# Kernel optimization log

Measured on AMD Instinct MI355X. Metric: run time of the kernel, lower is better.

The kernel has to match this reference:

```python
import jax, jax.numpy as jnp
import numpy as np

B, S = 32, 1
NUM_Q_HEADS, NUM_KV_HEADS, HEAD_DIM = 4, 2, 64
HIDDEN = NUM_Q_HEADS * HEAD_DIM          # 256
QKV_DIM = HIDDEN + 2 * NUM_KV_HEADS * HEAD_DIM  # 512
MAX_SEQ = 8192
G = NUM_Q_HEADS // NUM_KV_HEADS          # q heads per kv head


def setup_inputs() -> dict:
    key = jax.random.key(0)
    ks = jax.random.split(key, 6)
    x = jax.random.normal(ks[0], (B, S, HIDDEN), dtype=jnp.float32)
    kv_cache = jax.random.normal(ks[1], (B, 2, NUM_KV_HEADS, MAX_SEQ, HEAD_DIM), dtype=jnp.float32)
    ctx_len_tensor = jax.random.randint(ks[2], (B,), 0, 8000, dtype=jnp.int32)
    # RoPE table: [MAX_SEQ, HEAD_DIM] = [cos | sin] over half-dim
    half = HEAD_DIM // 2
    inv_freq = 1.0 / (10000.0 ** (np.arange(half, dtype=np.float32) / half))
    ang = np.arange(MAX_SEQ, dtype=np.float32)[:, None] * inv_freq[None, :]
    rope = jnp.asarray(np.concatenate([np.cos(ang), np.sin(ang)], axis=-1), dtype=jnp.float32)
    qkv_w = jax.random.normal(ks[3], (QKV_DIM, HIDDEN), dtype=jnp.float32) * (HIDDEN ** -0.5)
    qkv_b = jax.random.normal(ks[4], (QKV_DIM,), dtype=jnp.float32) * 0.02
    out_w = jax.random.normal(ks[5], (HIDDEN, HIDDEN), dtype=jnp.float32) * (HIDDEN ** -0.5)
    return {"x": x, "kv_cache": kv_cache, "ctx_len_tensor": ctx_len_tensor,
            "rope": rope, "qkv_w": qkv_w, "qkv_b": qkv_b, "out_w": out_w}


def reference(x, kv_cache, ctx_len_tensor, rope, qkv_w, qkv_b, out_w):
    b, s, _ = x.shape
    hd, half = HEAD_DIM, HEAD_DIM // 2
    qkv = jnp.einsum('bsd,ed->bse', x, qkv_w) + qkv_b
    q = qkv[..., :HIDDEN].reshape(b, s, NUM_Q_HEADS, hd)
    k = qkv[..., HIDDEN:HIDDEN + NUM_KV_HEADS * hd].reshape(b, s, NUM_KV_HEADS, hd)
    v = qkv[..., HIDDEN + NUM_KV_HEADS * hd:].reshape(b, s, NUM_KV_HEADS, hd)

    # positions of the new tokens in the cache
    pos = ctx_len_tensor[:, None] + jnp.arange(s)           # [b, s]
    cos = rope[pos, :half][:, :, None, :]                    # [b, s, 1, half]
    sin = rope[pos, half:][:, :, None, :]

    def rot(t):
        t1, t2 = t[..., :half], t[..., half:]
        return jnp.concatenate([t1 * cos - t2 * sin, t1 * sin + t2 * cos], axis=-1)

    q = rot(q)
    k = rot(k)

    # scatter new k/v into cache at pos (one-hot, positions distinct within batch)
    m = jnp.arange(MAX_SEQ)
    onehot = (m[None, None, :] == pos[:, :, None]).astype(kv_cache.dtype)   # [b, s, M]
    written = onehot.sum(axis=1)                                            # [b, M]
    keep = (1.0 - written)[:, None, :, None]                                # [b, 1, M, 1]
    cache_k = kv_cache[:, 0] * keep + jnp.einsum('bsm,bshd->bhmd', onehot, k)
    cache_v = kv_cache[:, 1] * keep + jnp.einsum('bsm,bshd->bhmd', onehot, v)

    # GQA decode attention over the updated cache (causal w.r.t. absolute position)
    qg = q.reshape(b, s, NUM_KV_HEADS, G, hd)
    scale = hd ** -0.5
    scores = jnp.einsum('bskgd,bkmd->bskgm', qg, cache_k) * scale           # [b,s,Hkv,G,M]
    valid = (m[None, None, :] <= pos[:, :, None])[:, :, None, None, :]
    scores = jnp.where(valid, scores, jnp.finfo(scores.dtype).min)
    attn = jax.nn.softmax(scores, axis=-1)
    ctx = jnp.einsum('bskgm,bkmd->bskgd', attn, cache_v).reshape(b, s, HIDDEN)

    out = jnp.einsum('bsd,ed->bse', ctx, out_w)
    updated_kv = jnp.stack([cache_k, cache_v], axis=1)
    return out, updated_kv
```

## Files before the change

### kernel.cpp

```cpp
#include <hip/hip_runtime.h>
#include <math.h>

#define B 32
#define NQH 4
#define NKVH 2
#define HD 64
#define HIDDEN 256
#define QKV_DIM 512
#define MAX_SEQ 8192
#define PLANE (MAX_SEQ * HD)
#define SCALE 0.125f
#define CH 256
#define NCH (MAX_SEQ / CH)
#define NEG_BIG -1e30f

typedef float f4 __attribute__((ext_vector_type(4)));

#define WS_K    8192
#define WS_V    12288
#define WS_PART 16384

__global__ __launch_bounds__(256) void qkv_rope_kernel(
    const float* __restrict__ x, const int* __restrict__ ctx_len,
    const float* __restrict__ rope, const float* __restrict__ qkv_w,
    const float* __restrict__ qkv_b, float* __restrict__ ws) {
    __shared__ float sx[HIDDEN];
    __shared__ float sv[HIDDEN];
    int bb = blockIdx.x;
    int b = bb >> 1, half = bb & 1;
    int tid = threadIdx.x;
    sx[tid] = x[b * HIDDEN + tid];
    __syncthreads();
    const float4* sx4 = (const float4*)sx;
    int e = half * 256 + tid;
    const float4* wrow = (const float4*)(qkv_w + e * HIDDEN);
    float acc = 0.f;
#pragma unroll 8
    for (int d4 = 0; d4 < HIDDEN / 4; ++d4) {
        float4 w = wrow[d4], xx = sx4[d4];
        acc += w.x * xx.x + w.y * xx.y + w.z * xx.z + w.w * xx.w;
    }
    sv[tid] = acc + qkv_b[e];
    __syncthreads();
    int pos = ctx_len[b];
    int nrot = half ? 64 : 128;
    if (tid < nrot) {
        int which = tid >> 5, d = tid & 31;
        float c = rope[pos * HD + d];
        float s = rope[pos * HD + 32 + d];
        int base = which * HD;
        float t1 = sv[base + d], t2 = sv[base + 32 + d];
        sv[base + d] = t1 * c - t2 * s;
        sv[base + 32 + d] = t1 * s + t2 * c;
    }
    __syncthreads();
    if (half == 0) {
        ws[b * HIDDEN + tid] = sv[tid];
    } else if (tid < 128) {
        ws[WS_K + b * 128 + tid] = sv[tid];
    } else {
        ws[WS_V + b * 128 + (tid - 128)] = sv[tid];
    }
}

__global__ __launch_bounds__(256) void fused_copy_attn(
    const float* __restrict__ kv_cache, const int* __restrict__ ctx_len,
    const float* __restrict__ ws, float* __restrict__ out_kv,
    float* __restrict__ partials) {
    int idx = blockIdx.x;
    int chunk = idx & (NCH - 1);
    int h = (idx >> 5) & 1;
    int b = idx >> 6;
    int pos = ctx_len[b];
    int start = chunk * CH;
    int tid = threadIdx.x;
    size_t koff = ((size_t)(b * 2 + 0) * NKVH + h) * PLANE;
    size_t voff = ((size_t)(b * 2 + 1) * NKVH + h) * PLANE;
    const f4* kin = (const f4*)(kv_cache + koff);
    const f4* vin = (const f4*)(kv_cache + voff);
    f4* kout = (f4*)(out_kv + koff);
    f4* vout = (f4*)(out_kv + voff);

    if (start >= pos) {
        int base = start * 16;
#pragma unroll
        for (int i = 0; i < 16; ++i) {
            int o = base + i * 256 + tid;
            f4 k4 = __builtin_nontemporal_load(&kin[o]);
            f4 v4 = __builtin_nontemporal_load(&vin[o]);
            __builtin_nontemporal_store(k4, &kout[o]);
            __builtin_nontemporal_store(v4, &vout[o]);
        }
        return;
    }

    int w = tid >> 6, lane = tid & 63;
    int g = lane >> 4, j = lane & 15;
    float4 q0 = *(const float4*)(ws + b * HIDDEN + (h * 2 + 0) * HD + 4 * j);
    float4 q1 = *(const float4*)(ws + b * HIDDEN + (h * 2 + 1) * HD + 4 * j);
    float m0 = NEG_BIG, m1 = NEG_BIG, l0 = 0.f, l1 = 0.f;
    float4 a0 = {0, 0, 0, 0}, a1 = {0, 0, 0, 0};
#pragma unroll 4
    for (int i = 0; i < CH / 16; ++i) {
        int row = start + i * 16 + w * 4 + g;
        int fidx = row * 16 + j;
        f4 k4 = __builtin_nontemporal_load(&kin[fidx]);
        f4 v4 = __builtin_nontemporal_load(&vin[fidx]);
        __builtin_nontemporal_store(k4, &kout[fidx]);
        __builtin_nontemporal_store(v4, &vout[fidx]);
        if (row < pos) {
            float s0 = q0.x * k4[0] + q0.y * k4[1] + q0.z * k4[2] + q0.w * k4[3];
            float s1 = q1.x * k4[0] + q1.y * k4[1] + q1.z * k4[2] + q1.w * k4[3];
#pragma unroll
            for (int off = 1; off <= 8; off <<= 1) {
                s0 += __shfl_xor(s0, off);
                s1 += __shfl_xor(s1, off);
            }
            s0 *= SCALE; s1 *= SCALE;
            float nm0 = fmaxf(m0, s0);
            float al0 = __expf(m0 - nm0);
            float p0 = __expf(s0 - nm0);
            l0 = l0 * al0 + p0;
            a0.x = a0.x * al0 + p0 * v4[0]; a0.y = a0.y * al0 + p0 * v4[1];
            a0.z = a0.z * al0 + p0 * v4[2]; a0.w = a0.w * al0 + p0 * v4[3];
            m0 = nm0;
            float nm1 = fmaxf(m1, s1);
            float al1 = __expf(m1 - nm1);
            float p1 = __expf(s1 - nm1);
            l1 = l1 * al1 + p1;
            a1.x = a1.x * al1 + p1 * v4[0]; a1.y = a1.y * al1 + p1 * v4[1];
            a1.z = a1.z * al1 + p1 * v4[2]; a1.w = a1.w * al1 + p1 * v4[3];
            m1 = nm1;
        }
    }
#pragma unroll
    for (int off = 16; off <= 32; off <<= 1) {
        float om0 = __shfl_xor(m0, off), ol0 = __shfl_xor(l0, off);
        float om1 = __shfl_xor(m1, off), ol1 = __shfl_xor(l1, off);
        float4 oa0, oa1;
        oa0.x = __shfl_xor(a0.x, off); oa0.y = __shfl_xor(a0.y, off);
        oa0.z = __shfl_xor(a0.z, off); oa0.w = __shfl_xor(a0.w, off);
        oa1.x = __shfl_xor(a1.x, off); oa1.y = __shfl_xor(a1.y, off);
        oa1.z = __shfl_xor(a1.z, off); oa1.w = __shfl_xor(a1.w, off);
        float M0 = fmaxf(m0, om0);
        float ea0 = __expf(m0 - M0), eb0 = __expf(om0 - M0);
        l0 = l0 * ea0 + ol0 * eb0;
        a0.x = a0.x * ea0 + oa0.x * eb0; a0.y = a0.y * ea0 + oa0.y * eb0;
        a0.z = a0.z * ea0 + oa0.z * eb0; a0.w = a0.w * ea0 + oa0.w * eb0;
        m0 = M0;
        float M1 = fmaxf(m1, om1);
        float ea1 = __expf(m1 - M1), eb1 = __expf(om1 - M1);
        l1 = l1 * ea1 + ol1 * eb1;
        a1.x = a1.x * ea1 + oa1.x * eb1; a1.y = a1.y * ea1 + oa1.y * eb1;
        a1.z = a1.z * ea1 + oa1.z * eb1; a1.w = a1.w * ea1 + oa1.w * eb1;
        m1 = M1;
    }
    __shared__ float sm[4][2], sl[4][2], sacc[4][2][64];
    if (lane < 16) {
        *(float4*)&sacc[w][0][4 * j] = a0;
        *(float4*)&sacc[w][1][4 * j] = a1;
        if (j == 0) { sm[w][0] = m0; sm[w][1] = m1; sl[w][0] = l0; sl[w][1] = l1; }
    }
    __syncthreads();
    if (tid < 128) {
        int gg = tid >> 6, d = tid & 63;
        float M = fmaxf(fmaxf(sm[0][gg], sm[1][gg]), fmaxf(sm[2][gg], sm[3][gg]));
        float L = 0.f, A = 0.f;
#pragma unroll
        for (int ww = 0; ww < 4; ++ww) {
            float e = __expf(sm[ww][gg] - M);
            L += sl[ww][gg] * e;
            A += sacc[ww][gg][d] * e;
        }
        float* ent = partials + (size_t)((b * 2 + h) * NCH + chunk) * 132;
        if (d == 0) { ent[gg] = M; ent[2 + gg] = L; }
        ent[4 + gg * 64 + d] = A;
    }
}

__global__ __launch_bounds__(256) void combine_proj_kernel(
    const int* __restrict__ ctx_len, const float* __restrict__ ws,
    const float* __restrict__ out_w, float* __restrict__ out_kv,
    float* __restrict__ out) {
    int b = blockIdx.x;
    int tid = threadIdx.x;
    int qh = tid >> 6, d = tid & 63;
    int h = qh >> 1, g = qh & 1;
    int pos = ctx_len[b];
    {
        int kv = tid >> 7, hh = (tid >> 6) & 1, dd = tid & 63;
        float nv = ws[(kv ? WS_V : WS_K) + b * 128 + hh * HD + dd];
        out_kv[((size_t)(b * 2 + kv) * NKVH + hh) * PLANE + (size_t)pos * HD + dd] = nv;
    }
    float qv = ws[b * HIDDEN + qh * HD + d];
    float kn = ws[WS_K + b * 128 + h * HD + d];
    float vn = ws[WS_V + b * 128 + h * HD + d];
    float s = qv * kn;
#pragma unroll
    for (int off = 32; off; off >>= 1) s += __shfl_xor(s, off);
    s *= SCALE;
    int nch = (pos + CH - 1) / CH;
    const float* pbase = ws + WS_PART + (size_t)(b * 2 + h) * NCH * 132;
    float M = s;
    for (int c = 0; c < nch; ++c) M = fmaxf(M, pbase[c * 132 + g]);
    float e0 = __expf(s - M);
    float L = e0;
    float A = e0 * vn;
    for (int c = 0; c < nch; ++c) {
        const float* ent = pbase + c * 132;
        float e = __expf(ent[g] - M);
        L += ent[2 + g] * e;
        A += ent[4 + g * 64 + d] * e;
    }
    __shared__ float sc[HIDDEN];
    sc[tid] = A / L;
    __syncthreads();
    const float4* wrow = (const float4*)(out_w + tid * HIDDEN);
    const float4* s4 = (const float4*)sc;
    float acc = 0.f;
#pragma unroll 8
    for (int d4 = 0; d4 < HIDDEN / 4; ++d4) {
        float4 w = wrow[d4], xx = s4[d4];
        acc += w.x * xx.x + w.y * xx.y + w.z * xx.z + w.w * xx.w;
    }
    out[b * HIDDEN + tid] = acc;
}

extern "C" void kernel_launch(void* const* d_in, const int* in_sizes, int n_in,
                              void* d_out, int out_size, void* d_ws, size_t ws_size,
                              hipStream_t stream) {
    const float* x = (const float*)d_in[0];
    const float* kv = (const float*)d_in[1];
    const int* cl = (const int*)d_in[2];
    const float* rope = (const float*)d_in[3];
    const float* qw = (const float*)d_in[4];
    const float* qb = (const float*)d_in[5];
    const float* ow = (const float*)d_in[6];
    float* out = (float*)d_out;
    float* out_kv = out + B * HIDDEN;
    float* ws = (float*)d_ws;

    qkv_rope_kernel<<<B * 2, 256, 0, stream>>>(x, cl, rope, qw, qb, ws);
    fused_copy_attn<<<B * NKVH * NCH, 256, 0, stream>>>(kv, cl, ws, out_kv, ws + WS_PART);
    combine_proj_kernel<<<B, 256, 0, stream>>>(cl, ws, ow, out_kv, out);
}
```

Measured before the change: 481.6 us.

## Fold QKV projection and RoPE into attention and combine kernels, dropping a launch

Removes the standalone qkv_rope kernel. Each attention block that has valid rows now recomputes its own two q heads (128 rows of the QKV GEMV plus RoPE) in shared memory. The combine kernel recomputes the full QKV projection per batch to get the new k/v and q. This saves one kernel launch and the dependency between the first two kernels, at the cost of redundant GEMV work repeated across many chunk blocks and extra weight reads.

```diff
diff --git a/kernel.cpp b/kernel.cpp
--- a/kernel.cpp
+++ b/kernel.cpp
@@ -16,57 +16,13 @@
 
 typedef float f4 __attribute__((ext_vector_type(4)));
 
-#define WS_K    8192
-#define WS_V    12288
 #define WS_PART 16384
 
-__global__ __launch_bounds__(256) void qkv_rope_kernel(
+__global__ __launch_bounds__(256) void fused_copy_attn(
     const float* __restrict__ x, const int* __restrict__ ctx_len,
     const float* __restrict__ rope, const float* __restrict__ qkv_w,
-    const float* __restrict__ qkv_b, float* __restrict__ ws) {
-    __shared__ float sx[HIDDEN];
-    __shared__ float sv[HIDDEN];
-    int bb = blockIdx.x;
-    int b = bb >> 1, half = bb & 1;
-    int tid = threadIdx.x;
-    sx[tid] = x[b * HIDDEN + tid];
-    __syncthreads();
-    const float4* sx4 = (const float4*)sx;
-    int e = half * 256 + tid;
-    const float4* wrow = (const float4*)(qkv_w + e * HIDDEN);
-    float acc = 0.f;
-#pragma unroll 8
-    for (int d4 = 0; d4 < HIDDEN / 4; ++d4) {
-        float4 w = wrow[d4], xx = sx4[d4];
-        acc += w.x * xx.x + w.y * xx.y + w.z * xx.z + w.w * xx.w;
-    }
-    sv[tid] = acc + qkv_b[e];
-    __syncthreads();
-    int pos = ctx_len[b];
-    int nrot = half ? 64 : 128;
-    if (tid < nrot) {
-        int which = tid >> 5, d = tid & 31;
-        float c = rope[pos * HD + d];
-        float s = rope[pos * HD + 32 + d];
-        int base = which * HD;
-        float t1 = sv[base + d], t2 = sv[base + 32 + d];
-        sv[base + d] = t1 * c - t2 * s;
-        sv[base + 32 + d] = t1 * s + t2 * c;
-    }
-    __syncthreads();
-    if (half == 0) {
-        ws[b * HIDDEN + tid] = sv[tid];
-    } else if (tid < 128) {
-        ws[WS_K + b * 128 + tid] = sv[tid];
-    } else {
-        ws[WS_V + b * 128 + (tid - 128)] = sv[tid];
-    }
-}
-
-__global__ __launch_bounds__(256) void fused_copy_attn(
-    const float* __restrict__ kv_cache, const int* __restrict__ ctx_len,
-    const float* __restrict__ ws, float* __restrict__ out_kv,
-    float* __restrict__ partials) {
+    const float* __restrict__ qkv_b, const float* __restrict__ kv_cache,
+    float* __restrict__ out_kv, float* __restrict__ partials) {
     int idx = blockIdx.x;
     int chunk = idx & (NCH - 1);
     int h = (idx >> 5) & 1;
@@ -94,10 +50,38 @@
         return;
     }
 
+    __shared__ float sx[HIDDEN];
+    __shared__ float sq[2 * HD];
+    sx[tid] = x[b * HIDDEN + tid];
+    __syncthreads();
+    if (tid < 128) {
+        int e = h * 128 + tid;
+        const float4* wrow = (const float4*)(qkv_w + e * HIDDEN);
+        const float4* sx4 = (const float4*)sx;
+        float acc = 0.f;
+#pragma unroll 8
+        for (int d4 = 0; d4 < HIDDEN / 4; ++d4) {
+            float4 ww = wrow[d4], xx = sx4[d4];
+            acc += ww.x * xx.x + ww.y * xx.y + ww.z * xx.z + ww.w * xx.w;
+        }
+        sq[tid] = acc + qkv_b[e];
+    }
+    __syncthreads();
+    if (tid < 64) {
+        int which = tid >> 5, d = tid & 31;
+        float c = rope[pos * HD + d];
+        float s = rope[pos * HD + 32 + d];
+        int base = which * HD;
+        float t1 = sq[base + d], t2 = sq[base + 32 + d];
+        sq[base + d] = t1 * c - t2 * s;
+        sq[base + 32 + d] = t1 * s + t2 * c;
+    }
+    __syncthreads();
+
     int w = tid >> 6, lane = tid & 63;
     int g = lane >> 4, j = lane & 15;
-    float4 q0 = *(const float4*)(ws + b * HIDDEN + (h * 2 + 0) * HD + 4 * j);
-    float4 q1 = *(const float4*)(ws + b * HIDDEN + (h * 2 + 1) * HD + 4 * j);
+    float4 q0 = *(const float4*)&sq[0 * HD + 4 * j];
+    float4 q1 = *(const float4*)&sq[1 * HD + 4 * j];
     float m0 = NEG_BIG, m1 = NEG_BIG, l0 = 0.f, l1 = 0.f;
     float4 a0 = {0, 0, 0, 0}, a1 = {0, 0, 0, 0};
 #pragma unroll 4
@@ -179,28 +163,59 @@
 }
 
 __global__ __launch_bounds__(256) void combine_proj_kernel(
-    const int* __restrict__ ctx_len, const float* __restrict__ ws,
-    const float* __restrict__ out_w, float* __restrict__ out_kv,
+    const float* __restrict__ x, const int* __restrict__ ctx_len,
+    const float* __restrict__ rope, const float* __restrict__ qkv_w,
+    const float* __restrict__ qkv_b, const float* __restrict__ out_w,
+    const float* __restrict__ partials, float* __restrict__ out_kv,
     float* __restrict__ out) {
+    __shared__ float sx[HIDDEN];
+    __shared__ float sqkv[QKV_DIM];
     int b = blockIdx.x;
     int tid = threadIdx.x;
+    sx[tid] = x[b * HIDDEN + tid];
+    __syncthreads();
+    const float4* sx4 = (const float4*)sx;
+#pragma unroll
+    for (int r = 0; r < 2; ++r) {
+        int e = tid + r * 256;
+        const float4* wrow = (const float4*)(qkv_w + e * HIDDEN);
+        float acc = 0.f;
+#pragma unroll 8
+        for (int d4 = 0; d4 < HIDDEN / 4; ++d4) {
+            float4 ww = wrow[d4], xx = sx4[d4];
+            acc += ww.x * xx.x + ww.y * xx.y + ww.z * xx.z + ww.w * xx.w;
+        }
+        sqkv[e] = acc + qkv_b[e];
+    }
+    __syncthreads();
+    int pos = ctx_len[b];
+    if (tid < 192) {
+        int which = tid >> 5;
+        int d = tid & 31;
+        float c = rope[pos * HD + d];
+        float s = rope[pos * HD + 32 + d];
+        int base = (which < 4) ? which * HD : HIDDEN + (which - 4) * HD;
+        float t1 = sqkv[base + d], t2 = sqkv[base + 32 + d];
+        sqkv[base + d] = t1 * c - t2 * s;
+        sqkv[base + 32 + d] = t1 * s + t2 * c;
+    }
+    __syncthreads();
+    {
+        int kv = tid >> 7, hh = (tid >> 6) & 1, dd = tid & 63;
+        float nv = sqkv[HIDDEN + kv * 128 + hh * HD + dd];
+        out_kv[((size_t)(b * 2 + kv) * NKVH + hh) * PLANE + (size_t)pos * HD + dd] = nv;
+    }
     int qh = tid >> 6, d = tid & 63;
     int h = qh >> 1, g = qh & 1;
-    int pos = ctx_len[b];
-    {
-        int kv = tid >> 7, hh = (tid >> 6) & 1, dd = tid & 63;
-        float nv = ws[(kv ? WS_V : WS_K) + b * 128 + hh * HD + dd];
-        out_kv[((size_t)(b * 2 + kv) * NKVH + hh) * PLANE + (size_t)pos * HD + dd] = nv;
-    }
-    float qv = ws[b * HIDDEN + qh * HD + d];
-    float kn = ws[WS_K + b * 128 + h * HD + d];
-    float vn = ws[WS_V + b * 128 + h * HD + d];
+    float qv = sqkv[qh * HD + d];
+    float kn = sqkv[HIDDEN + h * HD + d];
+    float vn = sqkv[HIDDEN + 128 + h * HD + d];
     float s = qv * kn;
 #pragma unroll
     for (int off = 32; off; off >>= 1) s += __shfl_xor(s, off);
     s *= SCALE;
     int nch = (pos + CH - 1) / CH;
-    const float* pbase = ws + WS_PART + (size_t)(b * 2 + h) * NCH * 132;
+    const float* pbase = partials + (size_t)(b * 2 + h) * NCH * 132;
     float M = s;
     for (int c = 0; c < nch; ++c) M = fmaxf(M, pbase[c * 132 + g]);
     float e0 = __expf(s - M);
@@ -220,8 +235,8 @@
     float acc = 0.f;
 #pragma unroll 8
     for (int d4 = 0; d4 < HIDDEN / 4; ++d4) {
-        float4 w = wrow[d4], xx = s4[d4];
-        acc += w.x * xx.x + w.y * xx.y + w.z * xx.z + w.w * xx.w;
+        float4 ww = wrow[d4], xx = s4[d4];
+        acc += ww.x * xx.x + ww.y * xx.y + ww.z * xx.z + ww.w * xx.w;
     }
     out[b * HIDDEN + tid] = acc;
 }
@@ -240,7 +255,8 @@
     float* out_kv = out + B * HIDDEN;
     float* ws = (float*)d_ws;
 
-    qkv_rope_kernel<<<B * 2, 256, 0, stream>>>(x, cl, rope, qw, qb, ws);
-    fused_copy_attn<<<B * NKVH * NCH, 256, 0, stream>>>(kv, cl, ws, out_kv, ws + WS_PART);
-    combine_proj_kernel<<<B, 256, 0, stream>>>(cl, ws, ow, out_kv, out);
+    fused_copy_attn<<<B * NKVH * NCH, 256, 0, stream>>>(
+        x, cl, rope, qw, qb, kv, out_kv, ws + WS_PART);
+    combine_proj_kernel<<<B, 256, 0, stream>>>(
+        x, cl, rope, qw, qb, ow, ws + WS_PART, out_kv, out);
 }
```

Result: no change. 488.7 us (+1.5%).
